# Kernel optimization log

Hardware: AMD Instinct MI355X
Metric: run time of the kernel (lower is better)

The kernel has to match this reference:

```python
import jax, jax.numpy as jnp
import numpy as np

DIM = 512
HEADS = 8
DIM_HEAD = 64
INNER = HEADS * DIM_HEAD  # 512
TOPK_FRAC = 0.7
SCALE = DIM_HEAD ** -0.5


def setup_inputs() -> dict:
    key = jax.random.key(0)
    k1, k2, k3, k4 = jax.random.split(key, 4)
    B, N = 4, 1024
    x = jax.random.normal(k1, (B, N, DIM), dtype=jnp.float32)
    # nn.Linear(dim, inner*3, bias=False): weight [3*inner, dim]; store transposed for x @ W
    w_qkv = jax.random.normal(k2, (DIM, 3 * INNER), dtype=jnp.float32) * (DIM ** -0.5)
    # to_out Linear(inner, dim) with bias
    w_out = jax.random.normal(k3, (INNER, DIM), dtype=jnp.float32) * (INNER ** -0.5)
    b_out = jax.random.normal(k4, (DIM,), dtype=jnp.float32) * 0.01
    return {"x": x, "w_qkv": w_qkv, "w_out": w_out, "b_out": b_out}


def reference(x, w_qkv, w_out, b_out):
    B, N, _ = x.shape
    H, D = HEADS, DIM_HEAD
    qkv = x @ w_qkv  # [B, N, 3*INNER]
    q, k, v = jnp.split(qkv, 3, axis=-1)
    # 'b n (h d) -> b h n d'
    reshape = lambda t: t.reshape(B, N, H, D).transpose(0, 2, 1, 3)
    q, k, v = reshape(q), reshape(k), reshape(v)
    dots = jnp.einsum('bhid,bhjd->bhij', q, k) * SCALE  # [B, H, N, N]
    # per-row top-k masking (kNN attention)
    kk = int(N * TOPK_FRAC)
    _, idx = jax.lax.top_k(dots, kk)  # [B, H, N, kk]
    bi = jnp.arange(B)[:, None, None, None]
    hi = jnp.arange(H)[None, :, None, None]
    ii = jnp.arange(N)[None, None, :, None]
    mask = jnp.zeros_like(dots).at[bi, hi, ii, idx].set(1.0)
    dots = jnp.where(mask > 0, dots, jnp.float32(-jnp.inf))
    attn = jax.nn.softmax(dots, axis=-1)
    out = jnp.einsum('bhij,bhjd->bhid', attn, v)  # [B, H, N, D]
    out = out.transpose(0, 2, 1, 3).reshape(B, N, H * D)  # 'b h n d -> b n (h d)'
    return out @ w_out + b_out
```

## Files before the change

kernel.cpp:

```cpp
#include <hip/hip_runtime.h>
#include <cstddef>

#define B_      4
#define N_      1024
#define DIM_    512
#define H_      8
#define D_      64
#define INNER_  512
#define TRIPLE_ 1536
#define KK_     716
#define SCALE_  0.125f

typedef short bf16x8 __attribute__((ext_vector_type(8)));
typedef float f32x4  __attribute__((ext_vector_type(4)));
typedef unsigned short ushort_t;
typedef ushort_t us8 __attribute__((ext_vector_type(8)));

__device__ __forceinline__ unsigned short bf16_rne(float f) {
    unsigned u = __float_as_uint(f);
    return (unsigned short)((u + 0x7FFFu + ((u >> 16) & 1u)) >> 16);
}
__device__ __forceinline__ float bf16_f(unsigned short s) {
    return __uint_as_float((unsigned)s << 16);
}
__device__ __forceinline__ unsigned f2key(float f) {
    unsigned u = __float_as_uint(f);
    return u ^ ((u & 0x80000000u) ? 0xFFFFFFFFu : 0x80000000u);
}
__device__ __forceinline__ float key2f(unsigned k) {
    unsigned u = (k & 0x80000000u) ? (k ^ 0x80000000u) : ~k;
    return __uint_as_float(u);
}
__device__ __forceinline__ int wave_count(int lc) {
    int c = __popcll(__ballot(lc & 1));
    c += __popcll(__ballot(lc & 2)) << 1;
    c += __popcll(__ballot(lc & 4)) << 2;
    c += __popcll(__ballot(lc & 8)) << 3;
    c += __popcll(__ballot(lc & 16)) << 4;
    return c;
}
__device__ __forceinline__ int count_ge(const unsigned* key, unsigned kt) {
    int lc = 0;
#pragma unroll
    for (int m = 0; m < 16; ++m) lc += (key[m] >= kt) ? 1 : 0;
    return wave_count(lc);
}
__device__ __forceinline__ unsigned bisect_exact(const unsigned* key,
                                                 bool hlo, bool hhi,
                                                 float tlo, float thi) {
    unsigned klo = hlo ? f2key(tlo) : 0u;
    unsigned khi = hhi ? f2key(thi) : 0xFFFFFFFFu;
    while (khi - klo > 1u) {
        const unsigned km = klo + ((khi - klo) >> 1);
        const int c = count_ge(key, km);
        if (c >= KK_) { klo = km; if (c == KK_) break; }
        else khi = km;
    }
    return klo;
}
__device__ __forceinline__ void topk2(const unsigned* key0, const unsigned* key1,
                                      float mu0, float sg0, float mu1, float sg1,
                                      unsigned& out0, unsigned& out1) {
    bool done0 = false, done1 = false;
    float tlo0 = 0.f, thi0 = 0.f, tlo1 = 0.f, thi1 = 0.f;
    int   clo0 = 0,   chi0 = 0,   clo1 = 0,   chi1 = 0;
    bool  hlo0 = false, hhi0 = false, hlo1 = false, hhi1 = false;
    float t0 = mu0 - 0.52189f * sg0;
    float t1 = mu1 - 0.52189f * sg1;
    unsigned res0 = 0u, res1 = 0u;
    for (int it = 0; it < 10; ++it) {
        if (done0 & done1) break;
        const unsigned kt0 = f2key(t0);
        const unsigned kt1 = f2key(t1);
        int lc0 = 0, lc1 = 0;
#pragma unroll
        for (int m = 0; m < 16; ++m) {
            lc0 += (key0[m] >= kt0) ? 1 : 0;
            lc1 += (key1[m] >= kt1) ? 1 : 0;
        }
        const int c0 = wave_count(lc0);
        const int c1 = wave_count(lc1);
        if (!done0) {
            if (c0 == KK_) { res0 = kt0; done0 = true; }
            else {
                if (c0 > KK_) { tlo0 = t0; clo0 = c0; hlo0 = true; }
                else          { thi0 = t0; chi0 = c0; hhi0 = true; }
                float tn;
                if (hlo0 && hhi0) {
                    tn = tlo0 + (thi0 - tlo0) * ((float)(clo0 - KK_) / (float)(clo0 - chi0));
                } else {
                    const float z    = (t0 - mu0) / sg0;
                    const float dens = fmaxf(408.5f * __expf(-0.5f * z * z) / sg0, 1.f);
                    tn = t0 + (float)(c0 - KK_) / dens;
                }
                if (hlo0 && !(tn > tlo0)) tn = hhi0 ? 0.5f * (tlo0 + thi0) : tlo0 + 0.25f * sg0;
                if (hhi0 && !(tn < thi0)) tn = hlo0 ? 0.5f * (tlo0 + thi0) : thi0 - 0.25f * sg0;
                t0 = tn;
            }
        }
        if (!done1) {
            if (c1 == KK_) { res1 = kt1; done1 = true; }
            else {
                if (c1 > KK_) { tlo1 = t1; clo1 = c1; hlo1 = true; }
                else          { thi1 = t1; chi1 = c1; hhi1 = true; }
                float tn;
                if (hlo1 && hhi1) {
                    tn = tlo1 + (thi1 - tlo1) * ((float)(clo1 - KK_) / (float)(clo1 - chi1));
                } else {
                    const float z    = (t1 - mu1) / sg1;
                    const float dens = fmaxf(408.5f * __expf(-0.5f * z * z) / sg1, 1.f);
                    tn = t1 + (float)(c1 - KK_) / dens;
                }
                if (hlo1 && !(tn > tlo1)) tn = hhi1 ? 0.5f * (tlo1 + thi1) : tlo1 + 0.25f * sg1;
                if (hhi1 && !(tn < thi1)) tn = hlo1 ? 0.5f * (tlo1 + thi1) : thi1 - 0.25f * sg1;
                t1 = tn;
            }
        }
    }
    if (!done0) res0 = bisect_exact(key0, hlo0, hhi0, tlo0, thi0);
    if (!done1) res1 = bisect_exact(key1, hlo1, hhi1, tlo1, thi1);
    out0 = res0;
    out1 = res1;
}
__device__ __forceinline__ void split8(const float* __restrict__ src,
                                       bf16x8& h8, bf16x8& l8) {
    float4 a = *(const float4*)src;
    float4 b = *(const float4*)(src + 4);
    float v[8] = {a.x, a.y, a.z, a.w, b.x, b.y, b.z, b.w};
#pragma unroll
    for (int i = 0; i < 8; ++i) {
        ushort_t hb = bf16_rne(v[i]);
        h8[i] = (short)hb;
        l8[i] = (short)bf16_rne(v[i] - bf16_f(hb));
    }
}

__global__ __launch_bounds__(256) void conv_wT2(const float* __restrict__ Wq,
                                                const float* __restrict__ Wo,
                                                ushort_t* __restrict__ WqTh,
                                                ushort_t* __restrict__ WqTl,
                                                ushort_t* __restrict__ WoTh,
                                                ushort_t* __restrict__ WoTl) {
    __shared__ float tile[32][33];
    const bool isQ = blockIdx.x < 48;
    const int  nb  = (isQ ? blockIdx.x : blockIdx.x - 48) * 32;
    const int  kb  = blockIdx.y * 32;
    const int  Nn  = isQ ? TRIPLE_ : DIM_;
    const float* W = isQ ? Wq : Wo;
    ushort_t* Th   = isQ ? WqTh : WoTh;
    ushort_t* Tl   = isQ ? WqTl : WoTl;
    const int tx = threadIdx.x & 31, ty = threadIdx.x >> 5;
    for (int yy = ty; yy < 32; yy += 8)
        tile[yy][tx] = W[(size_t)(kb + yy) * Nn + nb + tx];
    __syncthreads();
    for (int yy = ty; yy < 32; yy += 8) {
        float v = tile[tx][yy];
        ushort_t hb = bf16_rne(v);
        size_t idx = (size_t)(nb + yy) * DIM_ + kb + tx;
        Th[idx] = hb;
        Tl[idx] = bf16_rne(v - bf16_f(hb));
    }
}

__global__ __launch_bounds__(256) void gemm_qkv_mfma(
    const float* __restrict__ X,
    const ushort_t* __restrict__ Wh, const ushort_t* __restrict__ Wl,
    ushort_t* __restrict__ Qh, ushort_t* __restrict__ Ql,
    ushort_t* __restrict__ Kh, ushort_t* __restrict__ Kl,
    ushort_t* __restrict__ Vt) {
    __shared__ ushort_t stile[4][4608];
    __shared__ ushort_t BshH[2][2048];
    __shared__ ushort_t BshL[2][2048];
    const int t = threadIdx.x, w = t >> 6, l = t & 63;
    const int ln = l & 15, quad = l >> 4;
    const int n0 = blockIdx.y * 64;
    const int m0 = blockIdx.x * 128 + w * 32;
    f32x4 acc[2][4] = {};
    {
        const size_t xrow0 = (size_t)(m0 + ln) * DIM_;
        const size_t xrow1 = (size_t)(m0 + 16 + ln) * DIM_;
        const int srow = t >> 2;
        const int sk   = (t & 3) << 3;
        const size_t gb = (size_t)(n0 + srow) * DIM_ + sk;
        us8 nh = *(const us8*)&Wh[gb];
        us8 nl = *(const us8*)&Wl[gb];
        *(us8*)&BshH[0][t * 8] = nh;
        *(us8*)&BshL[0][t * 8] = nl;
        int cur = 0;
        for (int k0 = 0; k0 < DIM_; k0 += 32) {
            const bool more = (k0 + 32) < DIM_;
            const size_t gnext = gb + (size_t)(more ? k0 + 32 : 0);
            nh = *(const us8*)&Wh[gnext];
            nl = *(const us8*)&Wl[gnext];
            __syncthreads();
            const int ko = k0 + quad * 8;
            bf16x8 ah0, al0, ah1, al1;
            split8(&X[xrow0 + ko], ah0, al0);
            split8(&X[xrow1 + ko], ah1, al1);
#pragma unroll
            for (int j = 0; j < 4; ++j) {
                const int slot = (((j << 4) + ln) << 5) + (quad << 3);
                bf16x8 bh = *(const bf16x8*)&BshH[cur][slot];
                bf16x8 bl = *(const bf16x8*)&BshL[cur][slot];
                acc[0][j] = __builtin_amdgcn_mfma_f32_16x16x32_bf16(ah0, bh, acc[0][j], 0, 0, 0);
                acc[0][j] = __builtin_amdgcn_mfma_f32_16x16x32_bf16(al0, bh, acc[0][j], 0, 0, 0);
                acc[0][j] = __builtin_amdgcn_mfma_f32_16x16x32_bf16(ah0, bl, acc[0][j], 0, 0, 0);
                acc[1][j] = __builtin_amdgcn_mfma_f32_16x16x32_bf16(ah1, bh, acc[1][j], 0, 0, 0);
                acc[1][j] = __builtin_amdgcn_mfma_f32_16x16x32_bf16(al1, bh, acc[1][j], 0, 0, 0);
                acc[1][j] = __builtin_amdgcn_mfma_f32_16x16x32_bf16(ah1, bl, acc[1][j], 0, 0, 0);
            }
            if (more) {
                *(us8*)&BshH[cur ^ 1][t * 8] = nh;
                *(us8*)&BshL[cur ^ 1][t * 8] = nl;
            }
            cur ^= 1;
        }
    }
    const int sec = n0 >> 9;
    const int h   = (n0 >> 6) & 7;
    ushort_t* tw  = stile[w];
    const int b = m0 >> 10, nnb = m0 & 1023;
    if (sec < 2) {
        ushort_t* Hp = sec ? Kh : Qh;
        ushort_t* Lp = sec ? Kl : Ql;
        const float qsc = sec ? 1.0f : SCALE_;
#pragma unroll
        for (int i = 0; i < 2; ++i)
#pragma unroll
            for (int j = 0; j < 4; ++j)
#pragma unroll
                for (int g = 0; g < 4; ++g) {
                    const float v = acc[i][j][g] * qsc;
                    const ushort_t hb = bf16_rne(v);
                    const ushort_t lb = bf16_rne(v - bf16_f(hb));
                    const int tok = i * 16 + quad * 4 + g;
                    const int d   = j * 16 + ln;
                    tw[tok * 72 + d]        = hb;
                    tw[2304 + tok * 72 + d] = lb;
                }
        __syncthreads();
        const size_t rowbase = ((size_t)(b * 8 + h) * 1024 + nnb) * 64;
        const int dd = (l & 7) * 8;
#pragma unroll
        for (int s = 0; s < 4; ++s) {
            const int tl = s * 8 + (l >> 3);
            const size_t off = rowbase + (size_t)tl * 64 + dd;
            *(us8*)&Hp[off] = *(const us8*)&tw[tl * 72 + dd];
            *(us8*)&Lp[off] = *(const us8*)&tw[2304 + tl * 72 + dd];
        }
    } else {
#pragma unroll
        for (int i = 0; i < 2; ++i)
#pragma unroll
            for (int j = 0; j < 4; ++j)
#pragma unroll
                for (int g = 0; g < 4; ++g)
                    tw[(j * 16 + ln) * 40 + i * 16 + quad * 4 + g] = bf16_rne(acc[i][j][g]);
        __syncthreads();
        const size_t vbase = (size_t)(b * 8 + h) * 65536 + nnb;
#pragma unroll
        for (int p = 0; p < 2; ++p) {
            const int d = (p << 5) + (l >> 1);
            const int c = (l & 1) << 4;
            ushort_t* dst = &Vt[vbase + (size_t)d * 1024 + c];
            *(us8*)dst       = *(const us8*)&tw[d * 40 + c];
            *(us8*)(dst + 8) = *(const us8*)&tw[d * 40 + c + 8];
        }
    }
}

__global__ __launch_bounds__(256) void gemm_out_mfma(
    const ushort_t* __restrict__ Ah, const ushort_t* __restrict__ Al,
    const ushort_t* __restrict__ Wh, const ushort_t* __restrict__ Wl,
    const float* __restrict__ bias, float* __restrict__ C) {
    __shared__ ushort_t BshH[2][2048];
    __shared__ ushort_t BshL[2][2048];
    const int t = threadIdx.x, w = t >> 6, l = t & 63;
    const int ln = l & 15, quad = l >> 4;
    const int n0 = blockIdx.y * 64;
    const int m0 = blockIdx.x * 128 + w * 32;
    f32x4 acc[2][4] = {};
    {
        const size_t arow0 = (size_t)(m0 + ln) * INNER_;
        const size_t arow1 = (size_t)(m0 + 16 + ln) * INNER_;
        const int srow = t >> 2;
        const int sk   = (t & 3) << 3;
        const size_t gb = (size_t)(n0 + srow) * INNER_ + sk;
        us8 nh = *(const us8*)&Wh[gb];
        us8 nl = *(const us8*)&Wl[gb];
        *(us8*)&BshH[0][t * 8] = nh;
        *(us8*)&BshL[0][t * 8] = nl;
        int cur = 0;
        for (int k0 = 0; k0 < INNER_; k0 += 32) {
            const bool more = (k0 + 32) < INNER_;
            const size_t gnext = gb + (size_t)(more ? k0 + 32 : 0);
            nh = *(const us8*)&Wh[gnext];
            nl = *(const us8*)&Wl[gnext];
            __syncthreads();
            const int ko = k0 + quad * 8;
            bf16x8 ah0 = *(const bf16x8*)&Ah[arow0 + ko];
            bf16x8 al0 = *(const bf16x8*)&Al[arow0 + ko];
            bf16x8 ah1 = *(const bf16x8*)&Ah[arow1 + ko];
            bf16x8 al1 = *(const bf16x8*)&Al[arow1 + ko];
#pragma unroll
            for (int j = 0; j < 4; ++j) {
                const int slot = (((j << 4) + ln) << 5) + (quad << 3);
                bf16x8 bh = *(const bf16x8*)&BshH[cur][slot];
                bf16x8 bl = *(const bf16x8*)&BshL[cur][slot];
                acc[0][j] = __builtin_amdgcn_mfma_f32_16x16x32_bf16(ah0, bh, acc[0][j], 0, 0, 0);
                acc[0][j] = __builtin_amdgcn_mfma_f32_16x16x32_bf16(al0, bh, acc[0][j], 0, 0, 0);
                acc[0][j] = __builtin_amdgcn_mfma_f32_16x16x32_bf16(ah0, bl, acc[0][j], 0, 0, 0);
                acc[1][j] = __builtin_amdgcn_mfma_f32_16x16x32_bf16(ah1, bh, acc[1][j], 0, 0, 0);
                acc[1][j] = __builtin_amdgcn_mfma_f32_16x16x32_bf16(al1, bh, acc[1][j], 0, 0, 0);
                acc[1][j] = __builtin_amdgcn_mfma_f32_16x16x32_bf16(ah1, bl, acc[1][j], 0, 0, 0);
            }
            if (more) {
                *(us8*)&BshH[cur ^ 1][t * 8] = nh;
                *(us8*)&BshL[cur ^ 1][t * 8] = nl;
            }
            cur ^= 1;
        }
    }
#pragma unroll
    for (int i = 0; i < 2; ++i)
#pragma unroll
        for (int j = 0; j < 4; ++j) {
            const int col = n0 + j * 16 + ln;
            const float bb = bias[col];
#pragma unroll
            for (int g = 0; g < 4; ++g) {
                const int token = m0 + i * 16 + quad * 4 + g;
                C[(size_t)token * DIM_ + col] = acc[i][j][g] + bb;
            }
        }
}

__global__ __launch_bounds__(512)
__attribute__((amdgpu_waves_per_eu(4, 4)))
void attn_mfma(const ushort_t* __restrict__ Qh,
               const ushort_t* __restrict__ Ql,
               const ushort_t* __restrict__ Kh,
               const ushort_t* __restrict__ Kl,
               const ushort_t* __restrict__ Vt,
               ushort_t* __restrict__ Oh,
               ushort_t* __restrict__ Ol) {
    __shared__ float sdots[16 * 1024];
    __shared__ float spartial[4][16][17];

    const int t    = threadIdx.x;
    const int w    = t >> 6;
    const int l    = t & 63;
    const int ln   = l & 15;
    const int quad = l >> 4;
    const int wg   = blockIdx.x;
    const int bh   = wg & 31;
    const int i0   = (wg >> 5) << 4;

    const size_t bhoff = (size_t)bh << 16;

    const ushort_t* qp  = Qh + bhoff + (size_t)(i0 + ln) * 64 + (quad << 3);
    const ushort_t* qlp = Ql + bhoff + (size_t)(i0 + ln) * 64 + (quad << 3);
    bf16x8 qh0 = *(const bf16x8*)qp;
    bf16x8 qh1 = *(const bf16x8*)(qp + 32);
    bf16x8 ql0 = *(const bf16x8*)qlp;
    bf16x8 ql1 = *(const bf16x8*)(qlp + 32);

    const int dblk  = w & 3;
    const int jbase = (w & 4) << 7;
    const ushort_t* vp =
        Vt + bhoff + (size_t)((dblk << 4) + ln) * 1024 + (quad << 3) + jbase;
    bf16x8 vpre[8];

    for (int tt = 0; tt < 8; ++tt) {
        const int j0 = ((w << 3) + tt) << 4;
        const ushort_t* kp  = Kh + bhoff + (size_t)(j0 + ln) * 64 + (quad << 3);
        const ushort_t* klp = Kl + bhoff + (size_t)(j0 + ln) * 64 + (quad << 3);
        bf16x8 kh0 = *(const bf16x8*)kp;
        bf16x8 kh1 = *(const bf16x8*)(kp + 32);
        bf16x8 kl0 = *(const bf16x8*)klp;
        bf16x8 kl1 = *(const bf16x8*)(klp + 32);
        f32x4 acc = {0.f, 0.f, 0.f, 0.f};
        acc = __builtin_amdgcn_mfma_f32_16x16x32_bf16(qh0, kh0, acc, 0, 0, 0);
        acc = __builtin_amdgcn_mfma_f32_16x16x32_bf16(qh1, kh1, acc, 0, 0, 0);
        acc = __builtin_amdgcn_mfma_f32_16x16x32_bf16(qh0, kl0, acc, 0, 0, 0);
        acc = __builtin_amdgcn_mfma_f32_16x16x32_bf16(qh1, kl1, acc, 0, 0, 0);
        acc = __builtin_amdgcn_mfma_f32_16x16x32_bf16(ql0, kh0, acc, 0, 0, 0);
        acc = __builtin_amdgcn_mfma_f32_16x16x32_bf16(ql1, kh1, acc, 0, 0, 0);
#pragma unroll
        for (int g = 0; g < 4; ++g) {
            const int row = (quad << 2) + g;
            sdots[(row << 10) + ((j0 + ln) ^ ((row & 7) << 2))] = acc[g];
        }
    }
    __syncthreads();

    ushort_t* sP = (ushort_t*)sdots;
    {
        const int r0 = w << 1, r1 = r0 | 1;
        const int swz0 = (r0 & 7) << 2, swz1 = (r1 & 7) << 2;
        const float* s0 = &sdots[r0 << 10];
        const float* s1 = &sdots[r1 << 10];
        unsigned key0[16], key1[16];
        float sa0 = 0.f, sb0 = 0.f, sa1 = 0.f, sb1 = 0.f;
#pragma unroll
        for (int m = 0; m < 4; ++m) {
            f32x4 kv0 = *(const f32x4*)&s0[((l << 2) + (m << 8)) ^ swz0];
            f32x4 kv1 = *(const f32x4*)&s1[((l << 2) + (m << 8)) ^ swz1];
#pragma unroll
            for (int i = 0; i < 4; ++i) {
                key0[(m << 2) + i] = f2key(kv0[i]);
                key1[(m << 2) + i] = f2key(kv1[i]);
                sa0 += kv0[i];
                sb0 += kv0[i] * kv0[i];
                sa1 += kv1[i];
                sb1 += kv1[i] * kv1[i];
            }
        }
#pragma unroll
        for (int off = 32; off; off >>= 1) {
            sa0 += __shfl_xor(sa0, off, 64);
            sb0 += __shfl_xor(sb0, off, 64);
            sa1 += __shfl_xor(sa1, off, 64);
            sb1 += __shfl_xor(sb1, off, 64);
        }
        const float mu0 = sa0 * (1.0f / 1024.f);
        const float sg0 = sqrtf(fmaxf(sb0 * (1.0f / 1024.f) - mu0 * mu0, 1e-20f));
        const float mu1 = sa1 * (1.0f / 1024.f);
        const float sg1 = sqrtf(fmaxf(sb1 * (1.0f / 1024.f) - mu1 * mu1, 1e-20f));

        unsigned res0, res1;
        topk2(key0, key1, mu0, sg0, mu1, sg1, res0, res1);

        const float thr0 = key2f(res0), thr1 = key2f(res1);
        float pv0[16], pv1[16];
        float ls0 = 0.f, ls1 = 0.f;
#pragma unroll
        for (int m = 0; m < 16; ++m) {
            float p0 = (key0[m] >= res0) ? __expf(key2f(key0[m]) - thr0) : 0.f;
            float p1 = (key1[m] >= res1) ? __expf(key2f(key1[m]) - thr1) : 0.f;
            pv0[m] = p0;
            pv1[m] = p1;
            ls0 += p0;
            ls1 += p1;
        }
#pragma unroll
        for (int p = 0; p < 8; ++p)
            vpre[p] = *(const bf16x8*)(vp + p * 32);
#pragma unroll
        for (int off = 32; off; off >>= 1) {
            ls0 += __shfl_xor(ls0, off, 64);
            ls1 += __shfl_xor(ls1, off, 64);
        }
        const float inv0 = 1.f / ls0, inv1 = 1.f / ls1;
#pragma unroll
        for (int m = 0; m < 4; ++m) {
            const int g0 = ((l >> 1) + (m << 5)) ^ (r0 & 7);
            const int g1 = ((l >> 1) + (m << 5)) ^ (r1 & 7);
            ushort4 pk0 = make_ushort4(bf16_rne(pv0[(m << 2) + 0] * inv0),
                                       bf16_rne(pv0[(m << 2) + 1] * inv0),
                                       bf16_rne(pv0[(m << 2) + 2] * inv0),
                                       bf16_rne(pv0[(m << 2) + 3] * inv0));
            ushort4 pk1 = make_ushort4(bf16_rne(pv1[(m << 2) + 0] * inv1),
                                       bf16_rne(pv1[(m << 2) + 1] * inv1),
                                       bf16_rne(pv1[(m << 2) + 2] * inv1),
                                       bf16_rne(pv1[(m << 2) + 3] * inv1));
            *(ushort4*)&sP[(r0 << 11) + (g0 << 3) + ((l & 1) << 2)] = pk0;
            *(ushort4*)&sP[(r1 << 11) + (g1 << 3) + ((l & 1) << 2)] = pk1;
        }
    }
    __syncthreads();

    const int prow = ln << 11;
    const int rsw  = ln & 7;
    bf16x8 vnx[8];
#pragma unroll
    for (int p = 0; p < 8; ++p)
        vnx[p] = *(const bf16x8*)(vp + 256 + p * 32);
    f32x4 oa[4] = {};
    __builtin_amdgcn_s_setprio(1);
#pragma unroll
    for (int p = 0; p < 8; ++p) {
        const int j0 = p * 32;
        const int g = ((jbase + j0) >> 3) + quad;
        bf16x8 af = *(const bf16x8*)&sP[prow + ((g ^ rsw) << 3)];
        oa[p & 3] = __builtin_amdgcn_mfma_f32_16x16x32_bf16(af, vpre[p], oa[p & 3], 0, 0, 0);
    }
#pragma unroll
    for (int p = 0; p < 8; ++p) {
        const int j0 = 256 + p * 32;
        const int g = ((jbase + j0) >> 3) + quad;
        bf16x8 af = *(const bf16x8*)&sP[prow + ((g ^ rsw) << 3)];
        oa[p & 3] = __builtin_amdgcn_mfma_f32_16x16x32_bf16(af, vnx[p], oa[p & 3], 0, 0, 0);
    }
    __builtin_amdgcn_s_setprio(0);
    f32x4 oacc = (oa[0] + oa[1]) + (oa[2] + oa[3]);

    if (w & 4) {
#pragma unroll
        for (int g = 0; g < 4; ++g)
            spartial[dblk][(quad << 2) + g][ln] = oacc[g];
    }
    __syncthreads();
    if (!(w & 4)) {
        const int b = bh >> 3, h = bh & 7;
        const size_t obase =
            ((size_t)(b << 10) + i0 + (quad << 2)) * 512 + (h << 6) + (dblk << 4) + ln;
#pragma unroll
        for (int g = 0; g < 4; ++g) {
            const float v = oacc[g] + spartial[dblk][(quad << 2) + g][ln];
            ushort_t hb = bf16_rne(v);
            Oh[obase + (size_t)g * 512] = hb;
            Ol[obase + (size_t)g * 512] = bf16_rne(v - bf16_f(hb));
        }
    }
}

extern "C" void kernel_launch(void* const* d_in, const int* in_sizes, int n_in,
                              void* d_out, int out_size, void* d_ws, size_t ws_size,
                              hipStream_t stream) {
    const float* x     = (const float*)d_in[0];
    const float* w_qkv = (const float*)d_in[1];
    const float* w_out = (const float*)d_in[2];
    const float* b_out = (const float*)d_in[3];
    float*       out   = (float*)d_out;

    const size_t ON  = (size_t)4096 * 512;
    const size_t WQT = (size_t)1536 * 512;
    const size_t WOT = (size_t)512 * 512;
    const size_t QK  = (size_t)32 * 1024 * 64;

    ushort_t* p    = (ushort_t*)d_ws;
    ushort_t* Oh   = p;            p += ON;
    ushort_t* Ol   = p;            p += ON;
    ushort_t* WqTh = p;            p += WQT;
    ushort_t* WqTl = p;            p += WQT;
    ushort_t* WoTh = p;            p += WOT;
    ushort_t* WoTl = p;            p += WOT;
    ushort_t* Qh   = p;            p += QK;
    ushort_t* Ql   = p;            p += QK;
    ushort_t* Kh   = p;            p += QK;
    ushort_t* Kl   = p;            p += QK;
    ushort_t* Vt   = p;            p += QK;

    conv_wT2<<<dim3(64, 16), 256, 0, stream>>>(w_qkv, w_out, WqTh, WqTl, WoTh, WoTl);

    gemm_qkv_mfma<<<dim3(4096 / 128, TRIPLE_ / 64), 256, 0, stream>>>(
        x, WqTh, WqTl, Qh, Ql, Kh, Kl, Vt);

    attn_mfma<<<dim3(B_ * H_ * (N_ / 16)), 512, 0, stream>>>(Qh, Ql, Kh, Kl, Vt, Oh, Ol);

    gemm_out_mfma<<<dim3(4096 / 128, DIM_ / 64), 256, 0, stream>>>(
        Oh, Ol, WoTh, WoTl, b_out, out);
}
```

Measured before the change: 222.7 us.

## Fuse row stats into QK epilogue, Illinois-style secant, hardware bf16 pack

```diff
diff --git a/kernel.cpp b/kernel.cpp
--- a/kernel.cpp
+++ b/kernel.cpp
@@ -13,6 +13,7 @@
 
 typedef short bf16x8 __attribute__((ext_vector_type(8)));
 typedef float f32x4  __attribute__((ext_vector_type(4)));
+typedef unsigned uu4 __attribute__((ext_vector_type(4)));
 typedef unsigned short ushort_t;
 typedef ushort_t us8 __attribute__((ext_vector_type(8)));
 
@@ -63,12 +64,13 @@
                                       unsigned& out0, unsigned& out1) {
     bool done0 = false, done1 = false;
     float tlo0 = 0.f, thi0 = 0.f, tlo1 = 0.f, thi1 = 0.f;
-    int   clo0 = 0,   chi0 = 0,   clo1 = 0,   chi1 = 0;
+    float cwl0 = 0.f, cwh0 = 0.f, cwl1 = 0.f, cwh1 = 0.f;
     bool  hlo0 = false, hhi0 = false, hlo1 = false, hhi1 = false;
+    int   side0 = 0, side1 = 0;
     float t0 = mu0 - 0.52189f * sg0;
     float t1 = mu1 - 0.52189f * sg1;
     unsigned res0 = 0u, res1 = 0u;
-    for (int it = 0; it < 10; ++it) {
+    for (int it = 0; it < 12; ++it) {
         if (done0 & done1) break;
         const unsigned kt0 = f2key(t0);
         const unsigned kt1 = f2key(t1);
@@ -83,11 +85,16 @@
         if (!done0) {
             if (c0 == KK_) { res0 = kt0; done0 = true; }
             else {
-                if (c0 > KK_) { tlo0 = t0; clo0 = c0; hlo0 = true; }
-                else          { thi0 = t0; chi0 = c0; hhi0 = true; }
+                if (c0 > KK_) {
+                    if (side0 == 1 && hhi0) cwh0 = KK_ + (cwh0 - KK_) * 0.5f;
+                    tlo0 = t0; cwl0 = (float)c0; hlo0 = true; side0 = 1;
+                } else {
+                    if (side0 == -1 && hlo0) cwl0 = KK_ + (cwl0 - KK_) * 0.5f;
+                    thi0 = t0; cwh0 = (float)c0; hhi0 = true; side0 = -1;
+                }
                 float tn;
                 if (hlo0 && hhi0) {
-                    tn = tlo0 + (thi0 - tlo0) * ((float)(clo0 - KK_) / (float)(clo0 - chi0));
+                    tn = tlo0 + (thi0 - tlo0) * ((cwl0 - KK_) / (cwl0 - cwh0));
                 } else {
                     const float z    = (t0 - mu0) / sg0;
                     const float dens = fmaxf(408.5f * __expf(-0.5f * z * z) / sg0, 1.f);
@@ -101,11 +108,16 @@
         if (!done1) {
             if (c1 == KK_) { res1 = kt1; done1 = true; }
             else {
-                if (c1 > KK_) { tlo1 = t1; clo1 = c1; hlo1 = true; }
-                else          { thi1 = t1; chi1 = c1; hhi1 = true; }
+                if (c1 > KK_) {
+                    if (side1 == 1 && hhi1) cwh1 = KK_ + (cwh1 - KK_) * 0.5f;
+                    tlo1 = t1; cwl1 = (float)c1; hlo1 = true; side1 = 1;
+                } else {
+                    if (side1 == -1 && hlo1) cwl1 = KK_ + (cwl1 - KK_) * 0.5f;
+                    thi1 = t1; cwh1 = (float)c1; hhi1 = true; side1 = -1;
+                }
                 float tn;
                 if (hlo1 && hhi1) {
-                    tn = tlo1 + (thi1 - tlo1) * ((float)(clo1 - KK_) / (float)(clo1 - chi1));
+                    tn = tlo1 + (thi1 - tlo1) * ((cwl1 - KK_) / (cwl1 - cwh1));
                 } else {
                     const float z    = (t1 - mu1) / sg1;
                     const float dens = fmaxf(408.5f * __expf(-0.5f * z * z) / sg1, 1.f);
@@ -346,6 +358,7 @@
                ushort_t* __restrict__ Ol) {
     __shared__ float sdots[16 * 1024];
     __shared__ float spartial[4][16][17];
+    __shared__ float sstats[8][16][2];
 
     const int t    = threadIdx.x;
     const int w    = t >> 6;
@@ -371,6 +384,10 @@
         Vt + bhoff + (size_t)((dblk << 4) + ln) * 1024 + (quad << 3) + jbase;
     bf16x8 vpre[8];
 
+    unsigned* sdotu = (unsigned*)sdots;
+
+    float sa4[4] = {0.f, 0.f, 0.f, 0.f};
+    float sb4[4] = {0.f, 0.f, 0.f, 0.f};
     for (int tt = 0; tt < 8; ++tt) {
         const int j0 = ((w << 3) + tt) << 4;
         const ushort_t* kp  = Kh + bhoff + (size_t)(j0 + ln) * 64 + (quad << 3);
@@ -389,7 +406,25 @@
 #pragma unroll
         for (int g = 0; g < 4; ++g) {
             const int row = (quad << 2) + g;
-            sdots[(row << 10) + ((j0 + ln) ^ ((row & 7) << 2))] = acc[g];
+            const float v = acc[g];
+            sa4[g] += v;
+            sb4[g] += v * v;
+            sdotu[(row << 10) + ((j0 + ln) ^ ((row & 7) << 2))] = f2key(v);
+        }
+    }
+#pragma unroll
+    for (int off = 8; off; off >>= 1) {
+#pragma unroll
+        for (int g = 0; g < 4; ++g) {
+            sa4[g] += __shfl_xor(sa4[g], off, 64);
+            sb4[g] += __shfl_xor(sb4[g], off, 64);
+        }
+    }
+    if (ln == 0) {
+#pragma unroll
+        for (int g = 0; g < 4; ++g) {
+            sstats[w][(quad << 2) + g][0] = sa4[g];
+            sstats[w][(quad << 2) + g][1] = sb4[g];
         }
     }
     __syncthreads();
@@ -398,30 +433,26 @@
     {
         const int r0 = w << 1, r1 = r0 | 1;
         const int swz0 = (r0 & 7) << 2, swz1 = (r1 & 7) << 2;
-        const float* s0 = &sdots[r0 << 10];
-        const float* s1 = &sdots[r1 << 10];
+        const unsigned* s0 = &sdotu[r0 << 10];
+        const unsigned* s1 = &sdotu[r1 << 10];
         unsigned key0[16], key1[16];
+#pragma unroll
+        for (int m = 0; m < 4; ++m) {
+            uu4 kv0 = *(const uu4*)&s0[((l << 2) + (m << 8)) ^ swz0];
+            uu4 kv1 = *(const uu4*)&s1[((l << 2) + (m << 8)) ^ swz1];
+#pragma unroll
+            for (int i = 0; i < 4; ++i) {
+                key0[(m << 2) + i] = kv0[i];
+                key1[(m << 2) + i] = kv1[i];
+            }
+        }
         float sa0 = 0.f, sb0 = 0.f, sa1 = 0.f, sb1 = 0.f;
 #pragma unroll
-        for (int m = 0; m < 4; ++m) {
-            f32x4 kv0 = *(const f32x4*)&s0[((l << 2) + (m << 8)) ^ swz0];
-            f32x4 kv1 = *(const f32x4*)&s1[((l << 2) + (m << 8)) ^ swz1];
-#pragma unroll
-            for (int i = 0; i < 4; ++i) {
-                key0[(m << 2) + i] = f2key(kv0[i]);
-                key1[(m << 2) + i] = f2key(kv1[i]);
-                sa0 += kv0[i];
-                sb0 += kv0[i] * kv0[i];
-                sa1 += kv1[i];
-                sb1 += kv1[i] * kv1[i];
-            }
-        }
-#pragma unroll
-        for (int off = 32; off; off >>= 1) {
-            sa0 += __shfl_xor(sa0, off, 64);
-            sb0 += __shfl_xor(sb0, off, 64);
-            sa1 += __shfl_xor(sa1, off, 64);
-            sb1 += __shfl_xor(sb1, off, 64);
+        for (int ww = 0; ww < 8; ++ww) {
+            sa0 += sstats[ww][r0][0];
+            sb0 += sstats[ww][r0][1];
+            sa1 += sstats[ww][r1][0];
+            sb1 += sstats[ww][r1][1];
         }
         const float mu0 = sa0 * (1.0f / 1024.f);
         const float sg0 = sqrtf(fmaxf(sb0 * (1.0f / 1024.f) - mu0 * mu0, 1e-20f));
@@ -456,16 +487,17 @@
         for (int m = 0; m < 4; ++m) {
             const int g0 = ((l >> 1) + (m << 5)) ^ (r0 & 7);
             const int g1 = ((l >> 1) + (m << 5)) ^ (r1 & 7);
-            ushort4 pk0 = make_ushort4(bf16_rne(pv0[(m << 2) + 0] * inv0),
-                                       bf16_rne(pv0[(m << 2) + 1] * inv0),
-                                       bf16_rne(pv0[(m << 2) + 2] * inv0),
-                                       bf16_rne(pv0[(m << 2) + 3] * inv0));
-            ushort4 pk1 = make_ushort4(bf16_rne(pv1[(m << 2) + 0] * inv1),
-                                       bf16_rne(pv1[(m << 2) + 1] * inv1),
-                                       bf16_rne(pv1[(m << 2) + 2] * inv1),
-                                       bf16_rne(pv1[(m << 2) + 3] * inv1));
-            *(ushort4*)&sP[(r0 << 11) + (g0 << 3) + ((l & 1) << 2)] = pk0;
-            *(ushort4*)&sP[(r1 << 11) + (g1 << 3) + ((l & 1) << 2)] = pk1;
+            unsigned a0, b0, a1, b1;
+            asm("v_cvt_pk_bf16_f32 %0, %1, %2" : "=v"(a0)
+                : "v"(pv0[(m << 2) + 0] * inv0), "v"(pv0[(m << 2) + 1] * inv0));
+            asm("v_cvt_pk_bf16_f32 %0, %1, %2" : "=v"(b0)
+                : "v"(pv0[(m << 2) + 2] * inv0), "v"(pv0[(m << 2) + 3] * inv0));
+            asm("v_cvt_pk_bf16_f32 %0, %1, %2" : "=v"(a1)
+                : "v"(pv1[(m << 2) + 0] * inv1), "v"(pv1[(m << 2) + 1] * inv1));
+            asm("v_cvt_pk_bf16_f32 %0, %1, %2" : "=v"(b1)
+                : "v"(pv1[(m << 2) + 2] * inv1), "v"(pv1[(m << 2) + 3] * inv1));
+            *(uint2*)&sP[(r0 << 11) + (g0 << 3) + ((l & 1) << 2)] = make_uint2(a0, b0);
+            *(uint2*)&sP[(r1 << 11) + (g1 << 3) + ((l & 1) << 2)] = make_uint2(a1, b1);
         }
     }
     __syncthreads();
```

Measured after the change: 229.4 us. +3.0%, slower.
